# Kernel tuning notes

Measured on AMD Instinct MI355X. Metric: run time of the kernel, lower is better.

Reference implementation:

```python
import jax, jax.numpy as jnp
import numpy as np

B, N = 64, 256
DV, DP, DT, DF = 2048, 8, 768, 512


def setup_inputs() -> dict:
    key = jax.random.key(0)
    ks = jax.random.split(key, 9)
    visual = jax.random.normal(ks[0], (B, N, DV), dtype=jnp.float32)
    position = jax.random.uniform(ks[1], (B, N, DP), dtype=jnp.float32)
    text = jax.random.normal(ks[2], (B, N, DT), dtype=jnp.float32)
    s = 0.02
    Wt = jax.random.normal(ks[3], (DT, DF), dtype=jnp.float32) * s
    bt = jnp.zeros((DF,), dtype=jnp.float32)
    Wo = jax.random.normal(ks[4], (DV + DP, DF), dtype=jnp.float32) * s
    bo = jnp.zeros((DF,), dtype=jnp.float32)
    Wa = jax.random.normal(ks[5], (DF, 1), dtype=jnp.float32) * s
    ba = jnp.zeros((1,), dtype=jnp.float32)
    return {"visual": visual, "position": position, "text": text,
            "Wt": Wt, "bt": bt, "Wo": Wo, "bo": bo, "Wa": Wa, "ba": ba}


def relative_positions(position):
    # position: [B, N, P]
    n = position.shape[1]
    eye = jnp.eye(n, dtype=position.dtype)  # replaces per-element torch.diag loops
    p1 = position[:, :, None, :]            # [B, N, 1, P] -> row copies
    p2 = position[:, None, :, :]            # [B, 1, N, P] -> col copies
    p3 = eye[None, :, :, None] * p1         # diag(position[b, :, p])
    return p1 - p2 + p3                     # [B, N, N, P]


def reference(visual, position, text, Wt, bt, Wo, bo, Wa, ba):
    # query from first text token
    query = jax.nn.gelu(text[:, 0, :] @ Wt + bt, approximate=False)  # [B, DF]
    rel = relative_positions(position).sum(axis=2)                   # [B, N, P]
    objects = jnp.concatenate((visual, rel), axis=-1)                # [B, N, DV+DP]
    proj = objects @ Wo + bo                                         # [B, N, DF]
    scores = proj * query[:, None, :]                                # gated fusion
    out = (scores @ Wa + ba)[..., 0]                                 # [B, N]
    return out
```

## Files before the change

### kernel.cpp

```cpp
#include <hip/hip_runtime.h>
#include <hip/hip_bf16.h>
#include <math.h>

#define B_   64
#define N_   256
#define DV_  2048
#define DP_  8
#define DT_  768
#define DF_  512
#define DK_  2056

#define WS_WT 0
#define WS_S  32768
#define WS_C  33280
#define WS_V  33344

__global__ __launch_bounds__(256) void kA(
    const float* __restrict__ pos,
    const float* __restrict__ text,
    const float* __restrict__ Wt,
    const float* __restrict__ bt,
    const float* __restrict__ Wa,
    float* __restrict__ wT,
    float* __restrict__ S)
{
    const int bq = blockIdx.x >> 4;
    const int fg = blockIdx.x & 15;
    const int t  = threadIdx.x;

    __shared__ float  tx[4][DT_];
    __shared__ float4 sred[4][32][8];
    __shared__ float  spos[4][8][DP_];

    #pragma unroll
    for (int bb = 0; bb < 4; ++bb)
        for (int k = t; k < DT_; k += 256)
            tx[bb][k] = text[(size_t)(bq * 4 + bb) * N_ * DT_ + k];

    if (fg == 0) {
        const int bb = t >> 6, lane = t & 63;
        const int d = lane & 7, g8 = lane >> 3;
        float s = 0.f;
        for (int i = g8; i < N_; i += 8)
            s += pos[(size_t)(bq * 4 + bb) * N_ * DP_ + i * DP_ + d];
        spos[bb][g8][d] = s;
    }
    __syncthreads();

    if (fg == 0 && t < 32) {
        const int bb = t >> 3, d = t & 7;
        float s = 0.f;
        #pragma unroll
        for (int g = 0; g < 8; ++g) s += spos[bb][g][d];
        S[(bq * 4 + bb) * DP_ + d] = s;
    }

    const int fq = t & 7;
    const int kc = t >> 3;
    const int f0 = fg * 32 + fq * 4;
    float4 a0 = make_float4(0.f, 0.f, 0.f, 0.f);
    float4 a1 = a0, a2 = a0, a3 = a0;
    const int kbase = kc * 24;
    #pragma unroll 4
    for (int j = 0; j < 24; ++j) {
        const int k = kbase + j;
        const float4 wv = *(const float4*)(Wt + (size_t)k * DF_ + f0);
        const float x0 = tx[0][k], x1 = tx[1][k], x2 = tx[2][k], x3 = tx[3][k];
        a0.x = fmaf(x0, wv.x, a0.x); a0.y = fmaf(x0, wv.y, a0.y);
        a0.z = fmaf(x0, wv.z, a0.z); a0.w = fmaf(x0, wv.w, a0.w);
        a1.x = fmaf(x1, wv.x, a1.x); a1.y = fmaf(x1, wv.y, a1.y);
        a1.z = fmaf(x1, wv.z, a1.z); a1.w = fmaf(x1, wv.w, a1.w);
        a2.x = fmaf(x2, wv.x, a2.x); a2.y = fmaf(x2, wv.y, a2.y);
        a2.z = fmaf(x2, wv.z, a2.z); a2.w = fmaf(x2, wv.w, a2.w);
        a3.x = fmaf(x3, wv.x, a3.x); a3.y = fmaf(x3, wv.y, a3.y);
        a3.z = fmaf(x3, wv.z, a3.z); a3.w = fmaf(x3, wv.w, a3.w);
    }
    sred[0][kc][fq] = a0;
    sred[1][kc][fq] = a1;
    sred[2][kc][fq] = a2;
    sred[3][kc][fq] = a3;
    __syncthreads();

    if (t < 32) {
        const int bb = t >> 3, fq2 = t & 7;
        float4 s = sred[bb][0][fq2];
        for (int k2 = 1; k2 < 32; ++k2) {
            const float4 p = sred[bb][k2][fq2];
            s.x += p.x; s.y += p.y; s.z += p.z; s.w += p.w;
        }
        const float sv[4] = {s.x, s.y, s.z, s.w};
        const int b = bq * 4 + bb;
        #pragma unroll
        for (int cc = 0; cc < 4; ++cc) {
            const int f = fg * 32 + fq2 * 4 + cc;
            const float z = sv[cc] + bt[f];
            const float ge = 0.5f * z * (1.f + erff(z * 0.70710678118654752f));
            wT[(size_t)f * B_ + b] = ge * Wa[f];
        }
    }
}

__global__ __launch_bounds__(256) void kB(
    const float* __restrict__ Wo,
    const float* __restrict__ bo,
    const float* __restrict__ ba,
    const float* __restrict__ wT,
    float* __restrict__ v,
    float* __restrict__ c)
{
    const int t = threadIdx.x;
    __shared__ float  wo[4][DF_];
    __shared__ float4 red[4][16][16];
    __shared__ float  sbo[DF_];
    __shared__ float4 cred[16][16];

    if (blockIdx.x < 514) {
        const int k0 = blockIdx.x * 4;
        {
            const float4* src = (const float4*)(Wo + (size_t)k0 * DF_);
            float4*       dst = (float4*)wo;
            dst[t]       = src[t];
            dst[t + 256] = src[t + 256];
        }
        __syncthreads();

        const int bq = t & 15;
        const int fg = t >> 4;
        float4 acc0 = make_float4(0.f, 0.f, 0.f, 0.f);
        float4 acc1 = acc0, acc2 = acc0, acc3 = acc0;
        const int fbase = fg * 32;
        #pragma unroll 4
        for (int j = 0; j < 32; ++j) {
            const int f = fbase + j;
            const float4 wv = *(const float4*)(wT + (size_t)f * B_ + 4 * bq);
            const float s0 = wo[0][f], s1 = wo[1][f], s2 = wo[2][f], s3 = wo[3][f];
            acc0.x = fmaf(s0, wv.x, acc0.x); acc0.y = fmaf(s0, wv.y, acc0.y);
            acc0.z = fmaf(s0, wv.z, acc0.z); acc0.w = fmaf(s0, wv.w, acc0.w);
            acc1.x = fmaf(s1, wv.x, acc1.x); acc1.y = fmaf(s1, wv.y, acc1.y);
            acc1.z = fmaf(s1, wv.z, acc1.z); acc1.w = fmaf(s1, wv.w, acc1.w);
            acc2.x = fmaf(s2, wv.x, acc2.x); acc2.y = fmaf(s2, wv.y, acc2.y);
            acc2.z = fmaf(s2, wv.z, acc2.z); acc2.w = fmaf(s2, wv.w, acc2.w);
            acc3.x = fmaf(s3, wv.x, acc3.x); acc3.y = fmaf(s3, wv.y, acc3.y);
            acc3.z = fmaf(s3, wv.z, acc3.z); acc3.w = fmaf(s3, wv.w, acc3.w);
        }
        red[0][fg][bq] = acc0;
        red[1][fg][bq] = acc1;
        red[2][fg][bq] = acc2;
        red[3][fg][bq] = acc3;
        __syncthreads();
        if (t < 64) {
            const int r = t >> 4, bq2 = t & 15;
            float4 s = red[r][0][bq2];
            #pragma unroll
            for (int g = 1; g < 16; ++g) {
                const float4 p = red[r][g][bq2];
                s.x += p.x; s.y += p.y; s.z += p.z; s.w += p.w;
            }
            const float sv[4] = {s.x, s.y, s.z, s.w};
            #pragma unroll
            for (int cc = 0; cc < 4; ++cc)
                v[(size_t)(4 * bq2 + cc) * DK_ + k0 + r] = sv[cc];
        }
    } else {
        for (int k = t; k < DF_; k += 256) sbo[k] = bo[k];
        __syncthreads();
        const int bq = t & 15;
        const int fh = t >> 4;
        float4 acc = make_float4(0.f, 0.f, 0.f, 0.f);
        for (int j = 0; j < 32; ++j) {
            const int f = fh * 32 + j;
            const float s = sbo[f];
            const float4 wv = *(const float4*)(wT + (size_t)f * B_ + 4 * bq);
            acc.x = fmaf(s, wv.x, acc.x);
            acc.y = fmaf(s, wv.y, acc.y);
            acc.z = fmaf(s, wv.z, acc.z);
            acc.w = fmaf(s, wv.w, acc.w);
        }
        cred[fh][bq] = acc;
        __syncthreads();
        if (fh == 0) {
            float4 s = cred[0][bq];
            #pragma unroll
            for (int h = 1; h < 16; ++h) {
                const float4 p = cred[h][bq];
                s.x += p.x; s.y += p.y; s.z += p.z; s.w += p.w;
            }
            const float sv[4] = {s.x, s.y, s.z, s.w};
            #pragma unroll
            for (int cc = 0; cc < 4; ++cc)
                c[4 * bq + cc] = sv[cc] + ba[0];
        }
    }
}

__global__ __launch_bounds__(256) void kC(
    const float* __restrict__ visual,
    const float* __restrict__ pos,
    const float* __restrict__ v,
    const float* __restrict__ S,
    const float* __restrict__ c,
    float* __restrict__ out)
{
    const int t    = threadIdx.x;
    const int wave = t >> 6;
    const int lane = t & 63;
    const int R0   = blockIdx.x * 8 + wave * 2;
    const int b    = R0 >> 8;
    const int i0   = R0 & 255;

    const float4* vb = (const float4*)(v + (size_t)b * DK_);
    const float4* v0 = (const float4*)(visual + ((size_t)b * N_ + i0) * DV_);

    float a0 = 0.f, a1 = 0.f;
    #pragma unroll
    for (int j = 0; j < 8; ++j) {
        const int idx = lane + 64 * j;
        const float4 wv = vb[idx];
        const float4 x0 = v0[idx];
        const float4 x1 = v0[idx + 512];
        a0 = fmaf(x0.x, wv.x, a0); a0 = fmaf(x0.y, wv.y, a0);
        a0 = fmaf(x0.z, wv.z, a0); a0 = fmaf(x0.w, wv.w, a0);
        a1 = fmaf(x1.x, wv.x, a1); a1 = fmaf(x1.y, wv.y, a1);
        a1 = fmaf(x1.z, wv.z, a1); a1 = fmaf(x1.w, wv.w, a1);
    }
    #pragma unroll
    for (int off = 1; off < 64; off <<= 1) {
        a0 += __shfl_xor(a0, off, 64);
        a1 += __shfl_xor(a1, off, 64);
    }

    if (lane < 2) {
        const float accq = (lane == 0) ? a0 : a1;
        const int i = i0 + lane;
        const float* v2 = v + (size_t)b * DK_ + DV_;
        const float* pr = pos + ((size_t)b * N_ + i) * DP_;
        const float* Sb = S + b * DP_;
        float pd = 0.f, sd = 0.f;
        #pragma unroll
        for (int d = 0; d < DP_; ++d) {
            pd = fmaf(pr[d], v2[d], pd);
            sd = fmaf(Sb[d], v2[d], sd);
        }
        out[(size_t)b * N_ + i] = accq + 257.f * pd - sd + c[b];
    }
}

extern "C" void kernel_launch(void* const* d_in, const int* in_sizes, int n_in,
                              void* d_out, int out_size, void* d_ws, size_t ws_size,
                              hipStream_t stream) {
    const float* visual   = (const float*)d_in[0];
    const float* position = (const float*)d_in[1];
    const float* text     = (const float*)d_in[2];
    const float* Wt       = (const float*)d_in[3];
    const float* bt       = (const float*)d_in[4];
    const float* Wo       = (const float*)d_in[5];
    const float* bo       = (const float*)d_in[6];
    const float* Wa       = (const float*)d_in[7];
    const float* ba       = (const float*)d_in[8];
    float* out = (float*)d_out;

    float* ws = (float*)d_ws;
    float* wT = ws + WS_WT;
    float* S  = ws + WS_S;
    float* c  = ws + WS_C;
    float* v  = ws + WS_V;

    kA<<<256, 256, 0, stream>>>(position, text, Wt, bt, Wa, wT, S);
    kB<<<515, 256, 0, stream>>>(Wo, bo, ba, wT, v, c);
    kC<<<2048, 256, 0, stream>>>(visual, position, v, S, c, out);
}
```

Before: 49.72 us.

## Retile query GEMV over eight batches and stage v in LDS for visual dot kernel

kA now handles 8 batches per block with 16 features, loading text as float4 and reducing partial sums in two stages, so each Wt load is reused across more batches. kC now processes 16 rows per block (4 per wave), stages the per-batch v vector in shared memory, and precomputes the position and bias correction terms once per row group. This halves kC's grid and is meant to cut redundant v reads and per-row scalar overhead. The cost is more registers per thread and fewer blocks in flight to hide memory latency.

```diff
diff --git a/kernel.cpp b/kernel.cpp
--- a/kernel.cpp
+++ b/kernel.cpp
@@ -24,75 +24,93 @@
     float* __restrict__ wT,
     float* __restrict__ S)
 {
-    const int bq = blockIdx.x >> 4;
-    const int fg = blockIdx.x & 15;
+    const int bq = blockIdx.x >> 5;
+    const int fg = blockIdx.x & 31;
     const int t  = threadIdx.x;
 
-    __shared__ float  tx[4][DT_];
-    __shared__ float4 sred[4][32][8];
-    __shared__ float  spos[4][8][DP_];
-
+    __shared__ float  tx[8][DT_];
+    __shared__ float4 sred[8][4][64];
+    __shared__ float4 sred2[8][4][9];
+    __shared__ float  spos[8][4][DP_];
+
+    {
+        const float4* base = (const float4*)text;
+        #pragma unroll
+        for (int r = 0; r < 6; ++r) {
+            const int idx = t + 256 * r;
+            const int bb  = idx / 192;
+            const int j   = idx - bb * 192;
+            ((float4*)tx[bb])[j] = base[(size_t)(bq * 8 + bb) * (N_ * DT_ / 4) + j];
+        }
+    }
+
+    if (fg == 0) {
+        const int bb = t >> 5, l = t & 31;
+        const int d = l & 7, g4 = l >> 3;
+        float s = 0.f;
+        for (int i = g4; i < N_; i += 4)
+            s += pos[(size_t)(bq * 8 + bb) * N_ * DP_ + i * DP_ + d];
+        spos[bb][g4][d] = s;
+    }
+    __syncthreads();
+
+    if (fg == 0 && t < 64) {
+        const int bb = t >> 3, d = t & 7;
+        S[(bq * 8 + bb) * DP_ + d] =
+            spos[bb][0][d] + spos[bb][1][d] + spos[bb][2][d] + spos[bb][3][d];
+    }
+
+    const int fq = t & 3;
+    const int kc = t >> 2;
+    const int f0 = fg * 16 + fq * 4;
+    float4 acc[8];
     #pragma unroll
-    for (int bb = 0; bb < 4; ++bb)
-        for (int k = t; k < DT_; k += 256)
-            tx[bb][k] = text[(size_t)(bq * 4 + bb) * N_ * DT_ + k];
-
-    if (fg == 0) {
-        const int bb = t >> 6, lane = t & 63;
-        const int d = lane & 7, g8 = lane >> 3;
-        float s = 0.f;
-        for (int i = g8; i < N_; i += 8)
-            s += pos[(size_t)(bq * 4 + bb) * N_ * DP_ + i * DP_ + d];
-        spos[bb][g8][d] = s;
-    }
-    __syncthreads();
-
-    if (fg == 0 && t < 32) {
-        const int bb = t >> 3, d = t & 7;
-        float s = 0.f;
-        #pragma unroll
-        for (int g = 0; g < 8; ++g) s += spos[bb][g][d];
-        S[(bq * 4 + bb) * DP_ + d] = s;
-    }
-
-    const int fq = t & 7;
-    const int kc = t >> 3;
-    const int f0 = fg * 32 + fq * 4;
-    float4 a0 = make_float4(0.f, 0.f, 0.f, 0.f);
-    float4 a1 = a0, a2 = a0, a3 = a0;
-    const int kbase = kc * 24;
+    for (int bb = 0; bb < 8; ++bb) acc[bb] = make_float4(0.f, 0.f, 0.f, 0.f);
+
+    const int kbase = kc * 12;
     #pragma unroll 4
-    for (int j = 0; j < 24; ++j) {
+    for (int j = 0; j < 12; ++j) {
         const int k = kbase + j;
         const float4 wv = *(const float4*)(Wt + (size_t)k * DF_ + f0);
-        const float x0 = tx[0][k], x1 = tx[1][k], x2 = tx[2][k], x3 = tx[3][k];
-        a0.x = fmaf(x0, wv.x, a0.x); a0.y = fmaf(x0, wv.y, a0.y);
-        a0.z = fmaf(x0, wv.z, a0.z); a0.w = fmaf(x0, wv.w, a0.w);
-        a1.x = fmaf(x1, wv.x, a1.x); a1.y = fmaf(x1, wv.y, a1.y);
-        a1.z = fmaf(x1, wv.z, a1.z); a1.w = fmaf(x1, wv.w, a1.w);
-        a2.x = fmaf(x2, wv.x, a2.x); a2.y = fmaf(x2, wv.y, a2.y);
-        a2.z = fmaf(x2, wv.z, a2.z); a2.w = fmaf(x2, wv.w, a2.w);
-        a3.x = fmaf(x3, wv.x, a3.x); a3.y = fmaf(x3, wv.y, a3.y);
-        a3.z = fmaf(x3, wv.z, a3.z); a3.w = fmaf(x3, wv.w, a3.w);
-    }
-    sred[0][kc][fq] = a0;
-    sred[1][kc][fq] = a1;
-    sred[2][kc][fq] = a2;
-    sred[3][kc][fq] = a3;
+        #pragma unroll
+        for (int bb = 0; bb < 8; ++bb) {
+            const float x = tx[bb][k];
+            acc[bb].x = fmaf(x, wv.x, acc[bb].x);
+            acc[bb].y = fmaf(x, wv.y, acc[bb].y);
+            acc[bb].z = fmaf(x, wv.z, acc[bb].z);
+            acc[bb].w = fmaf(x, wv.w, acc[bb].w);
+        }
+    }
+    #pragma unroll
+    for (int bb = 0; bb < 8; ++bb) sred[bb][fq][kc] = acc[bb];
     __syncthreads();
 
+    {
+        const int combo = t >> 3, rt = t & 7;
+        const int bb = combo >> 2, fq2 = combo & 3;
+        float4 s = sred[bb][fq2][rt];
+        #pragma unroll
+        for (int g = 1; g < 8; ++g) {
+            const float4 p = sred[bb][fq2][g * 8 + rt];
+            s.x += p.x; s.y += p.y; s.z += p.z; s.w += p.w;
+        }
+        sred2[bb][fq2][rt] = s;
+    }
+    __syncthreads();
+
     if (t < 32) {
-        const int bb = t >> 3, fq2 = t & 7;
-        float4 s = sred[bb][0][fq2];
-        for (int k2 = 1; k2 < 32; ++k2) {
-            const float4 p = sred[bb][k2][fq2];
+        const int bb = t >> 2, fq2 = t & 3;
+        float4 s = sred2[bb][fq2][0];
+        #pragma unroll
+        for (int g = 1; g < 8; ++g) {
+            const float4 p = sred2[bb][fq2][g];
             s.x += p.x; s.y += p.y; s.z += p.z; s.w += p.w;
         }
         const float sv[4] = {s.x, s.y, s.z, s.w};
-        const int b = bq * 4 + bb;
+        const int b = bq * 8 + bb;
         #pragma unroll
         for (int cc = 0; cc < 4; ++cc) {
-            const int f = fg * 32 + fq2 * 4 + cc;
+            const int f = fg * 16 + fq2 * 4 + cc;
             const float z = sv[cc] + bt[f];
             const float ge = 0.5f * z * (1.f + erff(z * 0.70710678118654752f));
             wT[(size_t)f * B_ + b] = ge * Wa[f];
@@ -204,44 +222,65 @@
     const int t    = threadIdx.x;
     const int wave = t >> 6;
     const int lane = t & 63;
-    const int R0   = blockIdx.x * 8 + wave * 2;
-    const int b    = R0 >> 8;
-    const int i0   = R0 & 255;
-
-    const float4* vb = (const float4*)(v + (size_t)b * DK_);
-    const float4* v0 = (const float4*)(visual + ((size_t)b * N_ + i0) * DV_);
-
-    float a0 = 0.f, a1 = 0.f;
+    const int b    = blockIdx.x >> 4;
+    const int i0   = (blockIdx.x & 15) << 4;
+
+    __shared__ float sv[DV_];
+    __shared__ float rc[16];
+
+    {
+        const float4* src = (const float4*)(v + (size_t)b * DK_);
+        float4* dst = (float4*)sv;
+        dst[t]       = src[t];
+        dst[t + 256] = src[t + 256];
+    }
+    if (t < 16) {
+        const float* v2 = v + (size_t)b * DK_ + DV_;
+        const float* pr = pos + ((size_t)b * N_ + i0 + t) * DP_;
+        const float* Sb = S + b * DP_;
+        float pd = 0.f, sd = 0.f;
+        #pragma unroll
+        for (int d = 0; d < DP_; ++d) {
+            pd = fmaf(pr[d], v2[d], pd);
+            sd = fmaf(Sb[d], v2[d], sd);
+        }
+        rc[t] = 257.f * pd - sd + c[b];
+    }
+    __syncthreads();
+
+    const int r0 = i0 + wave * 4;
+    const float4* v0  = (const float4*)(visual + ((size_t)b * N_ + r0) * DV_);
+    const float4* svb = (const float4*)sv;
+
+    float a0 = 0.f, a1 = 0.f, a2 = 0.f, a3 = 0.f;
     #pragma unroll
     for (int j = 0; j < 8; ++j) {
         const int idx = lane + 64 * j;
-        const float4 wv = vb[idx];
+        const float4 wv = svb[idx];
         const float4 x0 = v0[idx];
         const float4 x1 = v0[idx + 512];
+        const float4 x2 = v0[idx + 1024];
+        const float4 x3 = v0[idx + 1536];
         a0 = fmaf(x0.x, wv.x, a0); a0 = fmaf(x0.y, wv.y, a0);
         a0 = fmaf(x0.z, wv.z, a0); a0 = fmaf(x0.w, wv.w, a0);
         a1 = fmaf(x1.x, wv.x, a1); a1 = fmaf(x1.y, wv.y, a1);
         a1 = fmaf(x1.z, wv.z, a1); a1 = fmaf(x1.w, wv.w, a1);
+        a2 = fmaf(x2.x, wv.x, a2); a2 = fmaf(x2.y, wv.y, a2);
+        a2 = fmaf(x2.z, wv.z, a2); a2 = fmaf(x2.w, wv.w, a2);
+        a3 = fmaf(x3.x, wv.x, a3); a3 = fmaf(x3.y, wv.y, a3);
+        a3 = fmaf(x3.z, wv.z, a3); a3 = fmaf(x3.w, wv.w, a3);
     }
     #pragma unroll
     for (int off = 1; off < 64; off <<= 1) {
         a0 += __shfl_xor(a0, off, 64);
         a1 += __shfl_xor(a1, off, 64);
-    }
-
-    if (lane < 2) {
-        const float accq = (lane == 0) ? a0 : a1;
-        const int i = i0 + lane;
-        const float* v2 = v + (size_t)b * DK_ + DV_;
-        const float* pr = pos + ((size_t)b * N_ + i) * DP_;
-        const float* Sb = S + b * DP_;
-        float pd = 0.f, sd = 0.f;
-        #pragma unroll
-        for (int d = 0; d < DP_; ++d) {
-            pd = fmaf(pr[d], v2[d], pd);
-            sd = fmaf(Sb[d], v2[d], sd);
-        }
-        out[(size_t)b * N_ + i] = accq + 257.f * pd - sd + c[b];
+        a2 += __shfl_xor(a2, off, 64);
+        a3 += __shfl_xor(a3, off, 64);
+    }
+
+    if (lane < 4) {
+        const float accq = (lane == 0) ? a0 : (lane == 1) ? a1 : (lane == 2) ? a2 : a3;
+        out[(size_t)b * N_ + r0 + lane] = accq + rc[wave * 4 + lane];
     }
 }
 
@@ -267,5 +306,5 @@
 
     kA<<<256, 256, 0, stream>>>(position, text, Wt, bt, Wa, wT, S);
     kB<<<515, 256, 0, stream>>>(Wo, bo, ba, wT, v, c);
-    kC<<<2048, 256, 0, stream>>>(visual, position, v, S, c, out);
+    kC<<<1024, 256, 0, stream>>>(visual, position, v, S, c, out);
 }
```

Measured after the change: 58.40 us. 1.17x slower.

## Fuse three kernels into one cooperative persistent kernel with grid syncs

Applied to the files above, without the earlier changes.

Merges the three launches (query/GELU, weight-fold, visual dot) into a single cooperative kernel whose persistent blocks loop over work items, with grid.sync between phases. Intra-block reductions move from shared memory to wave shuffles, and the Wo phase now processes 2 rows per block instead of 4. The aim is to remove launch gaps and inter-kernel drain. In exchange it adds two grid-wide barriers and an occupancy query on the host every call.

```diff
diff --git a/kernel.cpp b/kernel.cpp
--- a/kernel.cpp
+++ b/kernel.cpp
@@ -1,6 +1,8 @@
 #include <hip/hip_runtime.h>
-#include <hip/hip_bf16.h>
+#include <hip/hip_cooperative_groups.h>
 #include <math.h>
+
+namespace cg = cooperative_groups;
 
 #define B_   64
 #define N_   256
@@ -15,233 +17,255 @@
 #define WS_C  33280
 #define WS_V  33344
 
-__global__ __launch_bounds__(256) void kA(
+
+__global__ __launch_bounds__(256) void fused(
+    const float* __restrict__ visual,
     const float* __restrict__ pos,
     const float* __restrict__ text,
     const float* __restrict__ Wt,
     const float* __restrict__ bt,
-    const float* __restrict__ Wa,
-    float* __restrict__ wT,
-    float* __restrict__ S)
-{
-    const int bq = blockIdx.x >> 4;
-    const int fg = blockIdx.x & 15;
-    const int t  = threadIdx.x;
-
-    __shared__ float  tx[4][DT_];
-    __shared__ float4 sred[4][32][8];
-    __shared__ float  spos[4][8][DP_];
-
-    #pragma unroll
-    for (int bb = 0; bb < 4; ++bb)
-        for (int k = t; k < DT_; k += 256)
-            tx[bb][k] = text[(size_t)(bq * 4 + bb) * N_ * DT_ + k];
-
-    if (fg == 0) {
-        const int bb = t >> 6, lane = t & 63;
-        const int d = lane & 7, g8 = lane >> 3;
-        float s = 0.f;
-        for (int i = g8; i < N_; i += 8)
-            s += pos[(size_t)(bq * 4 + bb) * N_ * DP_ + i * DP_ + d];
-        spos[bb][g8][d] = s;
-    }
-    __syncthreads();
-
-    if (fg == 0 && t < 32) {
-        const int bb = t >> 3, d = t & 7;
-        float s = 0.f;
-        #pragma unroll
-        for (int g = 0; g < 8; ++g) s += spos[bb][g][d];
-        S[(bq * 4 + bb) * DP_ + d] = s;
-    }
-
-    const int fq = t & 7;
-    const int kc = t >> 3;
-    const int f0 = fg * 32 + fq * 4;
-    float4 a0 = make_float4(0.f, 0.f, 0.f, 0.f);
-    float4 a1 = a0, a2 = a0, a3 = a0;
-    const int kbase = kc * 24;
-    #pragma unroll 4
-    for (int j = 0; j < 24; ++j) {
-        const int k = kbase + j;
-        const float4 wv = *(const float4*)(Wt + (size_t)k * DF_ + f0);
-        const float x0 = tx[0][k], x1 = tx[1][k], x2 = tx[2][k], x3 = tx[3][k];
-        a0.x = fmaf(x0, wv.x, a0.x); a0.y = fmaf(x0, wv.y, a0.y);
-        a0.z = fmaf(x0, wv.z, a0.z); a0.w = fmaf(x0, wv.w, a0.w);
-        a1.x = fmaf(x1, wv.x, a1.x); a1.y = fmaf(x1, wv.y, a1.y);
-        a1.z = fmaf(x1, wv.z, a1.z); a1.w = fmaf(x1, wv.w, a1.w);
-        a2.x = fmaf(x2, wv.x, a2.x); a2.y = fmaf(x2, wv.y, a2.y);
-        a2.z = fmaf(x2, wv.z, a2.z); a2.w = fmaf(x2, wv.w, a2.w);
-        a3.x = fmaf(x3, wv.x, a3.x); a3.y = fmaf(x3, wv.y, a3.y);
-        a3.z = fmaf(x3, wv.z, a3.z); a3.w = fmaf(x3, wv.w, a3.w);
-    }
-    sred[0][kc][fq] = a0;
-    sred[1][kc][fq] = a1;
-    sred[2][kc][fq] = a2;
-    sred[3][kc][fq] = a3;
-    __syncthreads();
-
-    if (t < 32) {
-        const int bb = t >> 3, fq2 = t & 7;
-        float4 s = sred[bb][0][fq2];
-        for (int k2 = 1; k2 < 32; ++k2) {
-            const float4 p = sred[bb][k2][fq2];
-            s.x += p.x; s.y += p.y; s.z += p.z; s.w += p.w;
-        }
-        const float sv[4] = {s.x, s.y, s.z, s.w};
-        const int b = bq * 4 + bb;
-        #pragma unroll
-        for (int cc = 0; cc < 4; ++cc) {
-            const int f = fg * 32 + fq2 * 4 + cc;
-            const float z = sv[cc] + bt[f];
-            const float ge = 0.5f * z * (1.f + erff(z * 0.70710678118654752f));
-            wT[(size_t)f * B_ + b] = ge * Wa[f];
-        }
-    }
-}
-
-__global__ __launch_bounds__(256) void kB(
     const float* __restrict__ Wo,
     const float* __restrict__ bo,
+    const float* __restrict__ Wa,
     const float* __restrict__ ba,
-    const float* __restrict__ wT,
+    float* __restrict__ wT,
+    float* __restrict__ S,
+    float* __restrict__ c,
     float* __restrict__ v,
-    float* __restrict__ c)
-{
-    const int t = threadIdx.x;
-    __shared__ float  wo[4][DF_];
-    __shared__ float4 red[4][16][16];
-    __shared__ float  sbo[DF_];
-    __shared__ float4 cred[16][16];
-
-    if (blockIdx.x < 514) {
-        const int k0 = blockIdx.x * 4;
-        {
-            const float4* src = (const float4*)(Wo + (size_t)k0 * DF_);
-            float4*       dst = (float4*)wo;
-            dst[t]       = src[t];
-            dst[t + 256] = src[t + 256];
-        }
-        __syncthreads();
-
-        const int bq = t & 15;
-        const int fg = t >> 4;
-        float4 acc0 = make_float4(0.f, 0.f, 0.f, 0.f);
-        float4 acc1 = acc0, acc2 = acc0, acc3 = acc0;
-        const int fbase = fg * 32;
-        #pragma unroll 4
-        for (int j = 0; j < 32; ++j) {
-            const int f = fbase + j;
-            const float4 wv = *(const float4*)(wT + (size_t)f * B_ + 4 * bq);
-            const float s0 = wo[0][f], s1 = wo[1][f], s2 = wo[2][f], s3 = wo[3][f];
-            acc0.x = fmaf(s0, wv.x, acc0.x); acc0.y = fmaf(s0, wv.y, acc0.y);
-            acc0.z = fmaf(s0, wv.z, acc0.z); acc0.w = fmaf(s0, wv.w, acc0.w);
-            acc1.x = fmaf(s1, wv.x, acc1.x); acc1.y = fmaf(s1, wv.y, acc1.y);
-            acc1.z = fmaf(s1, wv.z, acc1.z); acc1.w = fmaf(s1, wv.w, acc1.w);
-            acc2.x = fmaf(s2, wv.x, acc2.x); acc2.y = fmaf(s2, wv.y, acc2.y);
-            acc2.z = fmaf(s2, wv.z, acc2.z); acc2.w = fmaf(s2, wv.w, acc2.w);
-            acc3.x = fmaf(s3, wv.x, acc3.x); acc3.y = fmaf(s3, wv.y, acc3.y);
-            acc3.z = fmaf(s3, wv.z, acc3.z); acc3.w = fmaf(s3, wv.w, acc3.w);
-        }
-        red[0][fg][bq] = acc0;
-        red[1][fg][bq] = acc1;
-        red[2][fg][bq] = acc2;
-        red[3][fg][bq] = acc3;
-        __syncthreads();
-        if (t < 64) {
-            const int r = t >> 4, bq2 = t & 15;
-            float4 s = red[r][0][bq2];
-            #pragma unroll
-            for (int g = 1; g < 16; ++g) {
-                const float4 p = red[r][g][bq2];
-                s.x += p.x; s.y += p.y; s.z += p.z; s.w += p.w;
-            }
-            const float sv[4] = {s.x, s.y, s.z, s.w};
-            #pragma unroll
-            for (int cc = 0; cc < 4; ++cc)
-                v[(size_t)(4 * bq2 + cc) * DK_ + k0 + r] = sv[cc];
-        }
-    } else {
-        for (int k = t; k < DF_; k += 256) sbo[k] = bo[k];
-        __syncthreads();
-        const int bq = t & 15;
-        const int fh = t >> 4;
-        float4 acc = make_float4(0.f, 0.f, 0.f, 0.f);
-        for (int j = 0; j < 32; ++j) {
-            const int f = fh * 32 + j;
-            const float s = sbo[f];
-            const float4 wv = *(const float4*)(wT + (size_t)f * B_ + 4 * bq);
-            acc.x = fmaf(s, wv.x, acc.x);
-            acc.y = fmaf(s, wv.y, acc.y);
-            acc.z = fmaf(s, wv.z, acc.z);
-            acc.w = fmaf(s, wv.w, acc.w);
-        }
-        cred[fh][bq] = acc;
-        __syncthreads();
-        if (fh == 0) {
-            float4 s = cred[0][bq];
-            #pragma unroll
-            for (int h = 1; h < 16; ++h) {
-                const float4 p = cred[h][bq];
-                s.x += p.x; s.y += p.y; s.z += p.z; s.w += p.w;
-            }
-            const float sv[4] = {s.x, s.y, s.z, s.w};
-            #pragma unroll
-            for (int cc = 0; cc < 4; ++cc)
-                c[4 * bq + cc] = sv[cc] + ba[0];
-        }
-    }
-}
-
-__global__ __launch_bounds__(256) void kC(
-    const float* __restrict__ visual,
-    const float* __restrict__ pos,
-    const float* __restrict__ v,
-    const float* __restrict__ S,
-    const float* __restrict__ c,
     float* __restrict__ out)
 {
+    __shared__ __align__(16) char smem[15360];
     const int t    = threadIdx.x;
     const int wave = t >> 6;
     const int lane = t & 63;
-    const int R0   = blockIdx.x * 8 + wave * 2;
-    const int b    = R0 >> 8;
-    const int i0   = R0 & 255;
-
-    const float4* vb = (const float4*)(v + (size_t)b * DK_);
-    const float4* v0 = (const float4*)(visual + ((size_t)b * N_ + i0) * DV_);
-
-    float a0 = 0.f, a1 = 0.f;
-    #pragma unroll
-    for (int j = 0; j < 8; ++j) {
-        const int idx = lane + 64 * j;
-        const float4 wv = vb[idx];
-        const float4 x0 = v0[idx];
-        const float4 x1 = v0[idx + 512];
-        a0 = fmaf(x0.x, wv.x, a0); a0 = fmaf(x0.y, wv.y, a0);
-        a0 = fmaf(x0.z, wv.z, a0); a0 = fmaf(x0.w, wv.w, a0);
-        a1 = fmaf(x1.x, wv.x, a1); a1 = fmaf(x1.y, wv.y, a1);
-        a1 = fmaf(x1.z, wv.z, a1); a1 = fmaf(x1.w, wv.w, a1);
+    cg::grid_group grid = cg::this_grid();
+
+    {
+        float*  tx   = (float*)smem;
+        float4* swA  = (float4*)(smem + 12288);
+        float*  spos = (float*)(smem + 14336);
+
+        for (int vb = blockIdx.x; vb < 256; vb += gridDim.x) {
+            const int bq = vb >> 4;
+            const int fg = vb & 15;
+
+            #pragma unroll
+            for (int r = 0; r < 3; ++r) {
+                const int idx = t + 256 * r;
+                const int bb  = idx / 192;
+                const int j   = idx - bb * 192;
+                ((float4*)(tx + (size_t)bb * DT_))[j] =
+                    ((const float4*)text)[(size_t)(bq * 4 + bb) * (N_ * DT_ / 4) + j];
+            }
+            if (fg == 0 && t < 128) {
+                const int bb = t >> 5, l = t & 31, d = l & 7, g4 = l >> 3;
+                float s = 0.f;
+                for (int i = g4; i < N_; i += 4)
+                    s += pos[(size_t)(bq * 4 + bb) * N_ * DP_ + i * DP_ + d];
+                spos[bb * 32 + g4 * 8 + d] = s;
+            }
+            __syncthreads();
+            if (fg == 0 && t < 32) {
+                const int bb = t >> 3, d = t & 7;
+                S[(bq * 4 + bb) * DP_ + d] = spos[bb * 32 + d] + spos[bb * 32 + 8 + d]
+                                           + spos[bb * 32 + 16 + d] + spos[bb * 32 + 24 + d];
+            }
+
+            const int fq = t & 7;
+            const int kc = t >> 3;
+            const int f0 = fg * 32 + fq * 4;
+            float4 a0 = make_float4(0.f, 0.f, 0.f, 0.f);
+            float4 a1 = a0, a2 = a0, a3 = a0;
+            const int kbase = kc * 24;
+            #pragma unroll 4
+            for (int j = 0; j < 24; ++j) {
+                const int k = kbase + j;
+                const float4 wv = *(const float4*)(Wt + (size_t)k * DF_ + f0);
+                const float x0 = tx[0 * DT_ + k], x1 = tx[1 * DT_ + k];
+                const float x2 = tx[2 * DT_ + k], x3 = tx[3 * DT_ + k];
+                a0.x = fmaf(x0, wv.x, a0.x); a0.y = fmaf(x0, wv.y, a0.y);
+                a0.z = fmaf(x0, wv.z, a0.z); a0.w = fmaf(x0, wv.w, a0.w);
+                a1.x = fmaf(x1, wv.x, a1.x); a1.y = fmaf(x1, wv.y, a1.y);
+                a1.z = fmaf(x1, wv.z, a1.z); a1.w = fmaf(x1, wv.w, a1.w);
+                a2.x = fmaf(x2, wv.x, a2.x); a2.y = fmaf(x2, wv.y, a2.y);
+                a2.z = fmaf(x2, wv.z, a2.z); a2.w = fmaf(x2, wv.w, a2.w);
+                a3.x = fmaf(x3, wv.x, a3.x); a3.y = fmaf(x3, wv.y, a3.y);
+                a3.z = fmaf(x3, wv.z, a3.z); a3.w = fmaf(x3, wv.w, a3.w);
+            }
+            #pragma unroll
+            for (int m = 8; m <= 32; m <<= 1) {
+                a0.x += __shfl_xor(a0.x, m, 64); a0.y += __shfl_xor(a0.y, m, 64);
+                a0.z += __shfl_xor(a0.z, m, 64); a0.w += __shfl_xor(a0.w, m, 64);
+                a1.x += __shfl_xor(a1.x, m, 64); a1.y += __shfl_xor(a1.y, m, 64);
+                a1.z += __shfl_xor(a1.z, m, 64); a1.w += __shfl_xor(a1.w, m, 64);
+                a2.x += __shfl_xor(a2.x, m, 64); a2.y += __shfl_xor(a2.y, m, 64);
+                a2.z += __shfl_xor(a2.z, m, 64); a2.w += __shfl_xor(a2.w, m, 64);
+                a3.x += __shfl_xor(a3.x, m, 64); a3.y += __shfl_xor(a3.y, m, 64);
+                a3.z += __shfl_xor(a3.z, m, 64); a3.w += __shfl_xor(a3.w, m, 64);
+            }
+            if (lane < 8) {
+                swA[wave * 32 + lane * 4 + 0] = a0;
+                swA[wave * 32 + lane * 4 + 1] = a1;
+                swA[wave * 32 + lane * 4 + 2] = a2;
+                swA[wave * 32 + lane * 4 + 3] = a3;
+            }
+            __syncthreads();
+            if (t < 32) {
+                const int fq2 = t & 7, bb = t >> 3;
+                float4 s = swA[fq2 * 4 + bb];
+                #pragma unroll
+                for (int w = 1; w < 4; ++w) {
+                    const float4 p = swA[w * 32 + fq2 * 4 + bb];
+                    s.x += p.x; s.y += p.y; s.z += p.z; s.w += p.w;
+                }
+                const float sv[4] = {s.x, s.y, s.z, s.w};
+                const int b = bq * 4 + bb;
+                #pragma unroll
+                for (int cc = 0; cc < 4; ++cc) {
+                    const int f = fg * 32 + fq2 * 4 + cc;
+                    const float z = sv[cc] + bt[f];
+                    const float ge = 0.5f * z * (1.f + erff(z * 0.70710678118654752f));
+                    wT[(size_t)f * B_ + b] = ge * Wa[f];
+                }
+            }
+            __syncthreads();
+        }
     }
-    #pragma unroll
-    for (int off = 1; off < 64; off <<= 1) {
-        a0 += __shfl_xor(a0, off, 64);
-        a1 += __shfl_xor(a1, off, 64);
+
+    __threadfence();
+    grid.sync();
+
+    {
+        float*  wo  = (float*)smem;
+        float4* swB = (float4*)(smem + 4096);
+        float*  sbo = (float*)(smem + 6144);
+
+        for (int vb = blockIdx.x; vb < 1029; vb += gridDim.x) {
+            if (vb < 1028) {
+                const int k0 = vb * 2;
+                ((float4*)wo)[t] = ((const float4*)(Wo + (size_t)k0 * DF_))[t];
+                __syncthreads();
+
+                const int bq = t & 15;
+                const int fgi = t >> 4;
+                float4 acc0 = make_float4(0.f, 0.f, 0.f, 0.f);
+                float4 acc1 = acc0;
+                const int fbase = fgi * 32;
+                #pragma unroll 4
+                for (int j = 0; j < 32; ++j) {
+                    const int f = fbase + j;
+                    const float4 wv = *(const float4*)(wT + (size_t)f * B_ + 4 * bq);
+                    const float s0 = wo[f], s1 = wo[DF_ + f];
+                    acc0.x = fmaf(s0, wv.x, acc0.x); acc0.y = fmaf(s0, wv.y, acc0.y);
+                    acc0.z = fmaf(s0, wv.z, acc0.z); acc0.w = fmaf(s0, wv.w, acc0.w);
+                    acc1.x = fmaf(s1, wv.x, acc1.x); acc1.y = fmaf(s1, wv.y, acc1.y);
+                    acc1.z = fmaf(s1, wv.z, acc1.z); acc1.w = fmaf(s1, wv.w, acc1.w);
+                }
+                #pragma unroll
+                for (int m = 16; m <= 32; m <<= 1) {
+                    acc0.x += __shfl_xor(acc0.x, m, 64); acc0.y += __shfl_xor(acc0.y, m, 64);
+                    acc0.z += __shfl_xor(acc0.z, m, 64); acc0.w += __shfl_xor(acc0.w, m, 64);
+                    acc1.x += __shfl_xor(acc1.x, m, 64); acc1.y += __shfl_xor(acc1.y, m, 64);
+                    acc1.z += __shfl_xor(acc1.z, m, 64); acc1.w += __shfl_xor(acc1.w, m, 64);
+                }
+                if (lane < 16) {
+                    swB[wave * 32 + lane]      = acc0;
+                    swB[wave * 32 + 16 + lane] = acc1;
+                }
+                __syncthreads();
+                if (t < 32) {
+                    const int row = t >> 4, bq2 = t & 15;
+                    float4 s = swB[row * 16 + bq2];
+                    #pragma unroll
+                    for (int w = 1; w < 4; ++w) {
+                        const float4 p = swB[w * 32 + row * 16 + bq2];
+                        s.x += p.x; s.y += p.y; s.z += p.z; s.w += p.w;
+                    }
+                    const float sv[4] = {s.x, s.y, s.z, s.w};
+                    #pragma unroll
+                    for (int cc = 0; cc < 4; ++cc)
+                        v[(size_t)(4 * bq2 + cc) * DK_ + k0 + row] = sv[cc];
+                }
+                __syncthreads();
+            } else {
+                for (int k = t; k < DF_; k += 256) sbo[k] = bo[k];
+                __syncthreads();
+                const int bq = t & 15;
+                const int fh = t >> 4;
+                float4 acc = make_float4(0.f, 0.f, 0.f, 0.f);
+                for (int j = 0; j < 32; ++j) {
+                    const int f = fh * 32 + j;
+                    const float s = sbo[f];
+                    const float4 wv = *(const float4*)(wT + (size_t)f * B_ + 4 * bq);
+                    acc.x = fmaf(s, wv.x, acc.x); acc.y = fmaf(s, wv.y, acc.y);
+                    acc.z = fmaf(s, wv.z, acc.z); acc.w = fmaf(s, wv.w, acc.w);
+                }
+                #pragma unroll
+                for (int m = 16; m <= 32; m <<= 1) {
+                    acc.x += __shfl_xor(acc.x, m, 64); acc.y += __shfl_xor(acc.y, m, 64);
+                    acc.z += __shfl_xor(acc.z, m, 64); acc.w += __shfl_xor(acc.w, m, 64);
+                }
+                if (lane < 16) swB[wave * 32 + lane] = acc;
+                __syncthreads();
+                if (t < 16) {
+                    float4 s = swB[t];
+                    #pragma unroll
+                    for (int w = 1; w < 4; ++w) {
+                        const float4 p = swB[w * 32 + t];
+                        s.x += p.x; s.y += p.y; s.z += p.z; s.w += p.w;
+                    }
+                    const float sv[4] = {s.x, s.y, s.z, s.w};
+                    #pragma unroll
+                    for (int cc = 0; cc < 4; ++cc)
+                        c[4 * t + cc] = sv[cc] + ba[0];
+                }
+                __syncthreads();
+            }
+        }
     }
 
-    if (lane < 2) {
-        const float accq = (lane == 0) ? a0 : a1;
-        const int i = i0 + lane;
-        const float* v2 = v + (size_t)b * DK_ + DV_;
-        const float* pr = pos + ((size_t)b * N_ + i) * DP_;
-        const float* Sb = S + b * DP_;
-        float pd = 0.f, sd = 0.f;
+    __threadfence();
+    grid.sync();
+
+    for (int vb = blockIdx.x; vb < 2048; vb += gridDim.x) {
+        const int b  = vb >> 5;
+        const int r0 = ((vb & 31) << 3) + wave * 2;
+
+        const float4* vb4 = (const float4*)(v + (size_t)b * DK_);
+        const float4* v0  = (const float4*)(visual + ((size_t)b * N_ + r0) * DV_);
+
+        float a0 = 0.f, a1 = 0.f;
         #pragma unroll
-        for (int d = 0; d < DP_; ++d) {
-            pd = fmaf(pr[d], v2[d], pd);
-            sd = fmaf(Sb[d], v2[d], sd);
-        }
-        out[(size_t)b * N_ + i] = accq + 257.f * pd - sd + c[b];
+        for (int j = 0; j < 8; ++j) {
+            const int idx = lane + 64 * j;
+            const float4 wv = vb4[idx];
+            const float4 x0 = v0[idx];
+            const float4 x1 = v0[idx + 512];
+            a0 = fmaf(x0.x, wv.x, a0); a0 = fmaf(x0.y, wv.y, a0);
+            a0 = fmaf(x0.z, wv.z, a0); a0 = fmaf(x0.w, wv.w, a0);
+            a1 = fmaf(x1.x, wv.x, a1); a1 = fmaf(x1.y, wv.y, a1);
+            a1 = fmaf(x1.z, wv.z, a1); a1 = fmaf(x1.w, wv.w, a1);
+        }
+        #pragma unroll
+        for (int off = 1; off < 64; off <<= 1) {
+            a0 += __shfl_xor(a0, off, 64);
+            a1 += __shfl_xor(a1, off, 64);
+        }
+
+        if (lane < 2) {
+            const float accq = (lane == 0) ? a0 : a1;
+            const int i = r0 + lane;
+            const float* v2 = v + (size_t)b * DK_ + DV_;
+            const float* pr = pos + ((size_t)b * N_ + i) * DP_;
+            const float* Sb = S + b * DP_;
+            float pd = 0.f, sd = 0.f;
+            #pragma unroll
+            for (int d = 0; d < DP_; ++d) {
+                pd = fmaf(pr[d], v2[d], pd);
+                sd = fmaf(Sb[d], v2[d], sd);
+            }
+            out[(size_t)b * N_ + i] = accq + 257.f * pd - sd + c[b];
+        }
     }
 }
 
@@ -265,7 +289,16 @@
     float* c  = ws + WS_C;
     float* v  = ws + WS_V;
 
-    kA<<<256, 256, 0, stream>>>(position, text, Wt, bt, Wa, wT, S);
-    kB<<<515, 256, 0, stream>>>(Wo, bo, ba, wT, v, c);
-    kC<<<2048, 256, 0, stream>>>(visual, position, v, S, c, out);
+    int maxB = 0;
+    hipOccupancyMaxActiveBlocksPerMultiprocessor(&maxB, fused, 256, 0);
+    if (maxB < 1) maxB = 1;
+    int grid = maxB * 256;
+    if (grid > 2048) grid = 2048;
+
+    void* args[] = {
+        (void*)&visual, (void*)&position, (void*)&text, (void*)&Wt, (void*)&bt,
+        (void*)&Wo, (void*)&bo, (void*)&Wa, (void*)&ba,
+        (void*)&wT, (void*)&S, (void*)&c, (void*)&v, (void*)&out
+    };
+    hipLaunchCooperativeKernel((void*)fused, dim3(grid), dim3(256), args, 0, stream);
 }
```

New measurement: 157.9 us. +217.7%, slower.
